# Kernel tuning notes

Hardware: AMD Instinct MI355X
Metric: run time of the kernel (lower is better)

The kernel has to match this reference:

```python
import jax, jax.numpy as jnp
import numpy as np

N_NODES = 100000
N_EDGES = 1600000
IN_FEATS = 64
OUT_FEATS = 64


def setup_inputs() -> dict:
    key = jax.random.key(0)
    k1, k2, k3, k4, k5 = jax.random.split(key, 5)
    h = jax.random.normal(k1, (N_NODES, IN_FEATS), dtype=jnp.float32)
    weight = jax.random.normal(k2, (IN_FEATS, OUT_FEATS), dtype=jnp.float32) * (1.0 / np.sqrt(OUT_FEATS))
    norm = jax.random.uniform(k3, (N_NODES, 1), dtype=jnp.float32)
    src = jax.random.randint(k4, (N_EDGES,), 0, N_NODES, dtype=jnp.int32)
    dst = jax.random.randint(k5, (N_EDGES,), 0, N_NODES, dtype=jnp.int32)
    return {"h": h, "weight": weight, "norm": norm, "src": src, "dst": dst}


def reference(h, weight, norm, src, dst):
    # GCN linear: [N, in] @ [in, out] -> [N, out]
    hw = jnp.matmul(h, weight)
    # pre-scale by source norm
    hn = hw * norm
    # gather messages at edge sources, scatter-sum into destinations
    msgs = hn[src]  # [E, out]
    agg = jax.ops.segment_sum(msgs, dst, num_segments=h.shape[0])
    # post-scale by destination norm
    return agg * norm
```

## Files before the change

kernel.cpp:

```cpp
#include <hip/hip_runtime.h>

#define N_NODES 100000
#define N_EDGES 1600000
#define F 64
#define NPB 128
#define NB ((N_NODES + NPB - 1) / NPB)
#define CAP 2432
#define BLK_E 8192
#define NSPLIT ((N_EDGES + BLK_E - 1) / BLK_E)
#define EPT (BLK_E / 512)
#define GEMM_ROWS 128
#define NGEMM ((N_NODES + GEMM_ROWS - 1) / GEMM_ROWS)

typedef unsigned short ushort_t;
typedef unsigned int uint_t;
using bf16x8 = __attribute__((ext_vector_type(8))) short;
using f32x4  = __attribute__((ext_vector_type(4))) float;

__device__ __forceinline__ ushort_t f2bf(float x) {
    uint_t u = __float_as_uint(x);
    u += 0x7FFFu + ((u >> 16) & 1u);
    return (ushort_t)(u >> 16);
}
__device__ __forceinline__ float bflo(uint_t v) {
    return __uint_as_float(v << 16);
}
__device__ __forceinline__ float bfhi(uint_t v) {
    return __uint_as_float(v & 0xFFFF0000u);
}

__launch_bounds__(512)
__global__ void gemm_split_kernel(const float* __restrict__ h,
                                  const float* __restrict__ w,
                                  const float* __restrict__ norm,
                                  ushort_t* __restrict__ hn,
                                  const int* __restrict__ src,
                                  const int* __restrict__ dst,
                                  ushort_t* __restrict__ offtab,
                                  uint_t* __restrict__ seg) {
    __shared__ int hist[1024];
    __shared__ int cur[NB + 2];
    __shared__ int sc[512];
    const int t = threadIdx.x;

    if (blockIdx.x < NSPLIT) {
        const int e0 = blockIdx.x * BLK_E;
        const int n  = min(BLK_E, N_EDGES - e0);

        for (int i = t; i < 1024; i += 512) hist[i] = 0;
        __syncthreads();

        uint_t rec[EPT];
        short  bin[EPT];
#pragma unroll
        for (int j = 0; j < EPT; ++j) {
            const int idx = t + j * 512;
            if (idx < n) {
                const int d = dst[e0 + idx];
                const int s = src[e0 + idx];
                bin[j] = (short)(d >> 7);
                rec[j] = ((uint_t)s << 7) | (uint_t)(d & 127);
                atomicAdd(&hist[bin[j]], 1);
            } else {
                bin[j] = -1;
            }
        }
        __syncthreads();

        const int b0i = 2 * t;
        const int v0 = hist[b0i], v1 = hist[b0i + 1];
        const int ssum = v0 + v1;
        sc[t] = ssum;
        __syncthreads();
        int acc = ssum;
#pragma unroll
        for (int off = 1; off < 512; off <<= 1) {
            const int add = (t >= off) ? sc[t - off] : 0;
            __syncthreads();
            acc += add;
            sc[t] = acc;
            __syncthreads();
        }
        int run = acc - ssum;
        ushort_t* offrow = offtab + (size_t)blockIdx.x * (NB + 1);
        const int vj[2] = {v0, v1};
#pragma unroll
        for (int j = 0; j < 2; ++j) {
            const int b = b0i + j;
            if (b < NB) {
                offrow[b] = (ushort_t)run;
                cur[b] = run;
            } else if (b == NB) {
                offrow[NB] = (ushort_t)run;
            }
            run += vj[j];
        }
        __syncthreads();

        uint_t* myseg = seg + (size_t)blockIdx.x * BLK_E;
#pragma unroll
        for (int j = 0; j < EPT; ++j) {
            if (bin[j] >= 0) {
                const int p = atomicAdd(&cur[bin[j]], 1);
                myseg[p] = rec[j];
            }
        }
    } else {
        const int gb  = blockIdx.x - NSPLIT;
        const int wv  = t >> 6;
        const int l   = t & 63;
        const int lr  = l & 15;
        const int lk  = l >> 4;
        const int col = (wv & 3) * 16 + lr;
        const int r0  = gb * GEMM_ROWS + (wv >> 2) * 64;

        bf16x8 b0, b1;
#pragma unroll
        for (int j = 0; j < 8; ++j) {
            b0[j] = (short)f2bf(w[(lk * 8 + j) * F + col]);
            b1[j] = (short)f2bf(w[(32 + lk * 8 + j) * F + col]);
        }

        float4 hv[4][4];
#pragma unroll
        for (int tt = 0; tt < 4; ++tt) {
            const int r  = r0 + tt * 16 + lr;
            const int rl = min(r, N_NODES - 1);
            const float* hp = h + (size_t)rl * F + lk * 8;
            hv[tt][0] = *(const float4*)(hp);
            hv[tt][1] = *(const float4*)(hp + 4);
            hv[tt][2] = *(const float4*)(hp + 32);
            hv[tt][3] = *(const float4*)(hp + 36);
        }

        f32x4 accv[4];
#pragma unroll
        for (int tt = 0; tt < 4; ++tt) {
            bf16x8 a0, a1;
            a0[0] = (short)f2bf(hv[tt][0].x); a0[1] = (short)f2bf(hv[tt][0].y);
            a0[2] = (short)f2bf(hv[tt][0].z); a0[3] = (short)f2bf(hv[tt][0].w);
            a0[4] = (short)f2bf(hv[tt][1].x); a0[5] = (short)f2bf(hv[tt][1].y);
            a0[6] = (short)f2bf(hv[tt][1].z); a0[7] = (short)f2bf(hv[tt][1].w);
            a1[0] = (short)f2bf(hv[tt][2].x); a1[1] = (short)f2bf(hv[tt][2].y);
            a1[2] = (short)f2bf(hv[tt][2].z); a1[3] = (short)f2bf(hv[tt][2].w);
            a1[4] = (short)f2bf(hv[tt][3].x); a1[5] = (short)f2bf(hv[tt][3].y);
            a1[6] = (short)f2bf(hv[tt][3].z); a1[7] = (short)f2bf(hv[tt][3].w);

            f32x4 acc = {0.f, 0.f, 0.f, 0.f};
            acc = __builtin_amdgcn_mfma_f32_16x16x32_bf16(a0, b0, acc, 0, 0, 0);
            acc = __builtin_amdgcn_mfma_f32_16x16x32_bf16(a1, b1, acc, 0, 0, 0);
            accv[tt] = acc;
        }

#pragma unroll
        for (int tt = 0; tt < 4; ++tt) {
#pragma unroll
            for (int i2 = 0; i2 < 4; ++i2) {
                const int m = r0 + tt * 16 + lk * 4 + i2;
                if (m < N_NODES)
                    hn[(size_t)m * F + col] = f2bf(accv[tt][i2] * norm[m]);
            }
        }
    }
}

__launch_bounds__(512)
__global__ void gather_build_kernel(const ushort_t* __restrict__ offtab,
                                    const uint_t* __restrict__ seg,
                                    const ushort_t* __restrict__ hn,
                                    const float* __restrict__ norm,
                                    float* __restrict__ out) {
    __shared__ uint_t ebuf[CAP];
    __shared__ int    lsrc[CAP];
    __shared__ int    cnt[NPB];
    __shared__ int    beg[NPB];
    __shared__ int    cur[NPB];
    __shared__ int    sc[NPB];
    __shared__ int    sstart[NSPLIT];
    __shared__ int    sbase[NSPLIT];
    __shared__ int    slenA[NSPLIT];
    __shared__ int    scn[512];

    const int b = blockIdx.x;
    const int t = threadIdx.x;

    int slen_v = 0, sstart_v = 0;
    if (t < NSPLIT) {
        const ushort_t* row = offtab + (size_t)t * (NB + 1);
        sstart_v = row[b];
        slen_v   = row[b + 1] - sstart_v;
        sstart[t] = sstart_v;
        slenA[t]  = slen_v;
    }
    if (t < NPB) cnt[t] = 0;
    scn[t] = slen_v;
    __syncthreads();

    int acc = slen_v;
#pragma unroll
    for (int off = 1; off < 512; off <<= 1) {
        const int add = (t >= off) ? scn[t - off] : 0;
        __syncthreads();
        acc += add;
        scn[t] = acc;
        __syncthreads();
    }
    if (t < NSPLIT) sbase[t] = acc - slen_v;
    __syncthreads();
    const int n = min(scn[511], CAP);

    const int grp    = t >> 4;
    const int lane16 = t & 15;
    for (int s = grp; s < NSPLIT; s += 32) {
        const int len  = slenA[s];
        const int base = sbase[s];
        const uint_t* sp = seg + (size_t)s * BLK_E + sstart[s];
        for (int j = lane16; j < len; j += 16) {
            const int o = base + j;
            if (o < CAP) {
                const uint_t v = sp[j];
                ebuf[o] = v;
                atomicAdd(&cnt[v & 127u], 1);
            }
        }
    }
    __syncthreads();

    int acc2 = (t < NPB) ? cnt[t] : 0;
    if (t < NPB) sc[t] = acc2;
    __syncthreads();
#pragma unroll
    for (int off = 1; off < NPB; off <<= 1) {
        int add = 0;
        if (t < NPB && t >= off) add = sc[t - off];
        __syncthreads();
        if (t < NPB) { acc2 += add; sc[t] = acc2; }
        __syncthreads();
    }
    if (t < NPB) {
        const int e = acc2 - cnt[t];
        beg[t] = e;
        cur[t] = e;
    }
    __syncthreads();

    for (int i = t; i < n; i += 512) {
        const uint_t e = ebuf[i];
        const int p = atomicAdd(&cur[e & 127u], 1);
        lsrc[p] = (int)(e >> 7);
    }
    __syncthreads();

    const int wave = t >> 6;
    const int lane = t & 63;
    const int s = lane >> 4;
    const int c = lane & 15;

    for (int ld = wave; ld < NPB; ld += 8) {
        const int node = b * NPB + ld;
        if (node >= N_NODES) break;

        const int bg = beg[ld];
        const int en = bg + cnt[ld];

        float a0 = 0.f, a1 = 0.f, a2 = 0.f, a3 = 0.f;
        int i = bg;
        for (; i + 15 < en; i += 16) {
            const int sA = lsrc[i + s];
            const int sB = lsrc[i + 4 + s];
            const int sC = lsrc[i + 8 + s];
            const int sD = lsrc[i + 12 + s];
            const uint2 vA = *(const uint2*)(hn + (size_t)sA * F + 4 * c);
            const uint2 vB = *(const uint2*)(hn + (size_t)sB * F + 4 * c);
            const uint2 vC = *(const uint2*)(hn + (size_t)sC * F + 4 * c);
            const uint2 vD = *(const uint2*)(hn + (size_t)sD * F + 4 * c);
            a0 += bflo(vA.x) + bflo(vB.x) + bflo(vC.x) + bflo(vD.x);
            a1 += bfhi(vA.x) + bfhi(vB.x) + bfhi(vC.x) + bfhi(vD.x);
            a2 += bflo(vA.y) + bflo(vB.y) + bflo(vC.y) + bflo(vD.y);
            a3 += bfhi(vA.y) + bfhi(vB.y) + bfhi(vC.y) + bfhi(vD.y);
        }
        for (; i + 7 < en; i += 8) {
            const int sA = lsrc[i + s];
            const int sB = lsrc[i + 4 + s];
            const uint2 vA = *(const uint2*)(hn + (size_t)sA * F + 4 * c);
            const uint2 vB = *(const uint2*)(hn + (size_t)sB * F + 4 * c);
            a0 += bflo(vA.x) + bflo(vB.x);
            a1 += bfhi(vA.x) + bfhi(vB.x);
            a2 += bflo(vA.y) + bflo(vB.y);
            a3 += bfhi(vA.y) + bfhi(vB.y);
        }
        for (; i < en; i += 4) {
            const int e = i + s;
            if (e < en) {
                const int sv = lsrc[e];
                const uint2 v = *(const uint2*)(hn + (size_t)sv * F + 4 * c);
                a0 += bflo(v.x);
                a1 += bfhi(v.x);
                a2 += bflo(v.y);
                a3 += bfhi(v.y);
            }
        }

        a0 += __shfl_xor(a0, 16); a0 += __shfl_xor(a0, 32);
        a1 += __shfl_xor(a1, 16); a1 += __shfl_xor(a1, 32);
        a2 += __shfl_xor(a2, 16); a2 += __shfl_xor(a2, 32);
        a3 += __shfl_xor(a3, 16); a3 += __shfl_xor(a3, 32);

        if (s == 0) {
            const float nv = norm[node];
            float4 r;
            r.x = a0 * nv; r.y = a1 * nv; r.z = a2 * nv; r.w = a3 * nv;
            *(float4*)(out + (size_t)node * F + 4 * c) = r;
        }
    }
}

extern "C" void kernel_launch(void* const* d_in, const int* in_sizes, int n_in,
                              void* d_out, int out_size, void* d_ws, size_t ws_size,
                              hipStream_t stream) {
    const float* h    = (const float*)d_in[0];
    const float* w    = (const float*)d_in[1];
    const float* norm = (const float*)d_in[2];
    const int*   src  = (const int*)d_in[3];
    const int*   dst  = (const int*)d_in[4];
    float* out = (float*)d_out;

    char* ws = (char*)d_ws;
    ushort_t* hn     = (ushort_t*)ws;
    uint_t*   seg    = (uint_t*)(ws + 12800000);
    ushort_t* offtab = (ushort_t*)(ws + 12800000 + 6422528);

    gemm_split_kernel<<<NSPLIT + NGEMM, 512, 0, stream>>>(
        h, w, norm, hn, src, dst, offtab, seg);

    gather_build_kernel<<<NB, 512, 0, stream>>>(offtab, seg, hn, norm, out);
}
```

Measured before the change: 71.54 us.

## Reorder GCN to aggregate scaled features first, then apply weight GEMM

Uses linearity to move the weight matrix multiply after the edge aggregation. The first kernel now only scales h by norm and converts it to bf16, the gather sums those rows into a bf16 aggregate buffer, and a new third kernel does the MFMA GEMM and the destination-norm scaling. This takes the GEMM off the critical path of the first stage, but adds a third launch, a bf16 round trip of the aggregate through memory, and an extra bf16 rounding of the summed values before the multiply.

```diff
diff --git a/kernel.cpp b/kernel.cpp
--- a/kernel.cpp
+++ b/kernel.cpp
@@ -9,6 +9,7 @@
 #define BLK_E 8192
 #define NSPLIT ((N_EDGES + BLK_E - 1) / BLK_E)
 #define EPT (BLK_E / 512)
+#define NSCALE 782
 #define GEMM_ROWS 128
 #define NGEMM ((N_NODES + GEMM_ROWS - 1) / GEMM_ROWS)
 
@@ -30,14 +31,13 @@
 }
 
 __launch_bounds__(512)
-__global__ void gemm_split_kernel(const float* __restrict__ h,
-                                  const float* __restrict__ w,
-                                  const float* __restrict__ norm,
-                                  ushort_t* __restrict__ hn,
-                                  const int* __restrict__ src,
-                                  const int* __restrict__ dst,
-                                  ushort_t* __restrict__ offtab,
-                                  uint_t* __restrict__ seg) {
+__global__ void scale_split_kernel(const float* __restrict__ h,
+                                   const float* __restrict__ norm,
+                                   ushort_t* __restrict__ g,
+                                   const int* __restrict__ src,
+                                   const int* __restrict__ dst,
+                                   ushort_t* __restrict__ offtab,
+                                   uint_t* __restrict__ seg) {
     __shared__ int hist[1024];
     __shared__ int cur[NB + 2];
     __shared__ int sc[512];
@@ -106,59 +106,19 @@
             }
         }
     } else {
-        const int gb  = blockIdx.x - NSPLIT;
-        const int wv  = t >> 6;
-        const int l   = t & 63;
-        const int lr  = l & 15;
-        const int lk  = l >> 4;
-        const int col = (wv & 3) * 16 + lr;
-        const int r0  = gb * GEMM_ROWS + (wv >> 2) * 64;
-
-        bf16x8 b0, b1;
-#pragma unroll
-        for (int j = 0; j < 8; ++j) {
-            b0[j] = (short)f2bf(w[(lk * 8 + j) * F + col]);
-            b1[j] = (short)f2bf(w[(32 + lk * 8 + j) * F + col]);
-        }
-
-        float4 hv[4][4];
-#pragma unroll
-        for (int tt = 0; tt < 4; ++tt) {
-            const int r  = r0 + tt * 16 + lr;
-            const int rl = min(r, N_NODES - 1);
-            const float* hp = h + (size_t)rl * F + lk * 8;
-            hv[tt][0] = *(const float4*)(hp);
-            hv[tt][1] = *(const float4*)(hp + 4);
-            hv[tt][2] = *(const float4*)(hp + 32);
-            hv[tt][3] = *(const float4*)(hp + 36);
-        }
-
-        f32x4 accv[4];
-#pragma unroll
-        for (int tt = 0; tt < 4; ++tt) {
-            bf16x8 a0, a1;
-            a0[0] = (short)f2bf(hv[tt][0].x); a0[1] = (short)f2bf(hv[tt][0].y);
-            a0[2] = (short)f2bf(hv[tt][0].z); a0[3] = (short)f2bf(hv[tt][0].w);
-            a0[4] = (short)f2bf(hv[tt][1].x); a0[5] = (short)f2bf(hv[tt][1].y);
-            a0[6] = (short)f2bf(hv[tt][1].z); a0[7] = (short)f2bf(hv[tt][1].w);
-            a1[0] = (short)f2bf(hv[tt][2].x); a1[1] = (short)f2bf(hv[tt][2].y);
-            a1[2] = (short)f2bf(hv[tt][2].z); a1[3] = (short)f2bf(hv[tt][2].w);
-            a1[4] = (short)f2bf(hv[tt][3].x); a1[5] = (short)f2bf(hv[tt][3].y);
-            a1[6] = (short)f2bf(hv[tt][3].z); a1[7] = (short)f2bf(hv[tt][3].w);
-
-            f32x4 acc = {0.f, 0.f, 0.f, 0.f};
-            acc = __builtin_amdgcn_mfma_f32_16x16x32_bf16(a0, b0, acc, 0, 0, 0);
-            acc = __builtin_amdgcn_mfma_f32_16x16x32_bf16(a1, b1, acc, 0, 0, 0);
-            accv[tt] = acc;
-        }
-
-#pragma unroll
-        for (int tt = 0; tt < 4; ++tt) {
-#pragma unroll
-            for (int i2 = 0; i2 < 4; ++i2) {
-                const int m = r0 + tt * 16 + lk * 4 + i2;
-                if (m < N_NODES)
-                    hn[(size_t)m * F + col] = f2bf(accv[tt][i2] * norm[m]);
+        const int sb = blockIdx.x - NSPLIT;
+        const int base = sb * 8192 + t * 16;
+        if (base < N_NODES * F) {
+            const float nv = norm[base >> 6];
+            const float4* hp = (const float4*)(h + base);
+            uint2* gp = (uint2*)(g + base);
+#pragma unroll
+            for (int q = 0; q < 4; ++q) {
+                const float4 v = hp[q];
+                uint2 r;
+                r.x = (uint_t)f2bf(v.x * nv) | ((uint_t)f2bf(v.y * nv) << 16);
+                r.y = (uint_t)f2bf(v.z * nv) | ((uint_t)f2bf(v.w * nv) << 16);
+                gp[q] = r;
             }
         }
     }
@@ -167,9 +127,8 @@
 __launch_bounds__(512)
 __global__ void gather_build_kernel(const ushort_t* __restrict__ offtab,
                                     const uint_t* __restrict__ seg,
-                                    const ushort_t* __restrict__ hn,
-                                    const float* __restrict__ norm,
-                                    float* __restrict__ out) {
+                                    const ushort_t* __restrict__ g,
+                                    ushort_t* __restrict__ agg) {
     __shared__ uint_t ebuf[CAP];
     __shared__ int    lsrc[CAP];
     __shared__ int    cnt[NPB];
@@ -270,10 +229,10 @@
             const int sB = lsrc[i + 4 + s];
             const int sC = lsrc[i + 8 + s];
             const int sD = lsrc[i + 12 + s];
-            const uint2 vA = *(const uint2*)(hn + (size_t)sA * F + 4 * c);
-            const uint2 vB = *(const uint2*)(hn + (size_t)sB * F + 4 * c);
-            const uint2 vC = *(const uint2*)(hn + (size_t)sC * F + 4 * c);
-            const uint2 vD = *(const uint2*)(hn + (size_t)sD * F + 4 * c);
+            const uint2 vA = *(const uint2*)(g + (size_t)sA * F + 4 * c);
+            const uint2 vB = *(const uint2*)(g + (size_t)sB * F + 4 * c);
+            const uint2 vC = *(const uint2*)(g + (size_t)sC * F + 4 * c);
+            const uint2 vD = *(const uint2*)(g + (size_t)sD * F + 4 * c);
             a0 += bflo(vA.x) + bflo(vB.x) + bflo(vC.x) + bflo(vD.x);
             a1 += bfhi(vA.x) + bfhi(vB.x) + bfhi(vC.x) + bfhi(vD.x);
             a2 += bflo(vA.y) + bflo(vB.y) + bflo(vC.y) + bflo(vD.y);
@@ -282,8 +241,8 @@
         for (; i + 7 < en; i += 8) {
             const int sA = lsrc[i + s];
             const int sB = lsrc[i + 4 + s];
-            const uint2 vA = *(const uint2*)(hn + (size_t)sA * F + 4 * c);
-            const uint2 vB = *(const uint2*)(hn + (size_t)sB * F + 4 * c);
+            const uint2 vA = *(const uint2*)(g + (size_t)sA * F + 4 * c);
+            const uint2 vB = *(const uint2*)(g + (size_t)sB * F + 4 * c);
             a0 += bflo(vA.x) + bflo(vB.x);
             a1 += bfhi(vA.x) + bfhi(vB.x);
             a2 += bflo(vA.y) + bflo(vB.y);
@@ -293,7 +252,7 @@
             const int e = i + s;
             if (e < en) {
                 const int sv = lsrc[e];
-                const uint2 v = *(const uint2*)(hn + (size_t)sv * F + 4 * c);
+                const uint2 v = *(const uint2*)(g + (size_t)sv * F + 4 * c);
                 a0 += bflo(v.x);
                 a1 += bfhi(v.x);
                 a2 += bflo(v.y);
@@ -307,10 +266,55 @@
         a3 += __shfl_xor(a3, 16); a3 += __shfl_xor(a3, 32);
 
         if (s == 0) {
-            const float nv = norm[node];
-            float4 r;
-            r.x = a0 * nv; r.y = a1 * nv; r.z = a2 * nv; r.w = a3 * nv;
-            *(float4*)(out + (size_t)node * F + 4 * c) = r;
+            uint2 r;
+            r.x = (uint_t)f2bf(a0) | ((uint_t)f2bf(a1) << 16);
+            r.y = (uint_t)f2bf(a2) | ((uint_t)f2bf(a3) << 16);
+            *(uint2*)(agg + (size_t)node * F + 4 * c) = r;
+        }
+    }
+}
+
+__launch_bounds__(512)
+__global__ void gemm_out_kernel(const ushort_t* __restrict__ agg,
+                                const float* __restrict__ w,
+                                const float* __restrict__ norm,
+                                float* __restrict__ out) {
+    const int t   = threadIdx.x;
+    const int wv  = t >> 6;
+    const int l   = t & 63;
+    const int lr  = l & 15;
+    const int lk  = l >> 4;
+    const int col = (wv & 3) * 16 + lr;
+    const int r0  = blockIdx.x * GEMM_ROWS + (wv >> 2) * 64;
+
+    bf16x8 b0, b1;
+#pragma unroll
+    for (int j = 0; j < 8; ++j) {
+        b0[j] = (short)f2bf(w[(lk * 8 + j) * F + col]);
+        b1[j] = (short)f2bf(w[(32 + lk * 8 + j) * F + col]);
+    }
+
+    f32x4 accv[4];
+#pragma unroll
+    for (int tt = 0; tt < 4; ++tt) {
+        const int r  = r0 + tt * 16 + lr;
+        const int rl = min(r, N_NODES - 1);
+        const bf16x8 a0 = *(const bf16x8*)(agg + (size_t)rl * F + lk * 8);
+        const bf16x8 a1 = *(const bf16x8*)(agg + (size_t)rl * F + 32 + lk * 8);
+
+        f32x4 acc = {0.f, 0.f, 0.f, 0.f};
+        acc = __builtin_amdgcn_mfma_f32_16x16x32_bf16(a0, b0, acc, 0, 0, 0);
+        acc = __builtin_amdgcn_mfma_f32_16x16x32_bf16(a1, b1, acc, 0, 0, 0);
+        accv[tt] = acc;
+    }
+
+#pragma unroll
+    for (int tt = 0; tt < 4; ++tt) {
+#pragma unroll
+        for (int i2 = 0; i2 < 4; ++i2) {
+            const int m = r0 + tt * 16 + lk * 4 + i2;
+            if (m < N_NODES)
+                out[(size_t)m * F + col] = accv[tt][i2] * norm[m];
         }
     }
 }
@@ -326,12 +330,15 @@
     float* out = (float*)d_out;
 
     char* ws = (char*)d_ws;
-    ushort_t* hn     = (ushort_t*)ws;
-    uint_t*   seg    = (uint_t*)(ws + 12800000);
-    ushort_t* offtab = (ushort_t*)(ws + 12800000 + 6422528);
-
-    gemm_split_kernel<<<NSPLIT + NGEMM, 512, 0, stream>>>(
-        h, w, norm, hn, src, dst, offtab, seg);
-
-    gather_build_kernel<<<NB, 512, 0, stream>>>(offtab, seg, hn, norm, out);
-}
+    ushort_t* g      = (ushort_t*)ws;
+    ushort_t* agg    = (ushort_t*)(ws + 12800000);
+    uint_t*   seg    = (uint_t*)(ws + 25600000);
+    ushort_t* offtab = (ushort_t*)(ws + 25600000 + 6422528);
+
+    scale_split_kernel<<<NSPLIT + NSCALE, 512, 0, stream>>>(
+        h, norm, g, src, dst, offtab, seg);
+
+    gather_build_kernel<<<NB, 512, 0, stream>>>(offtab, seg, g, agg);
+
+    gemm_out_kernel<<<NGEMM, 512, 0, stream>>>(agg, w, norm, out);
+}
```

New measurement: 79.39 us. 1.11x slower.
